# Optimization experiments

Measured on AMD Instinct MI355X. Metric: run time of the kernel, lower is better.

Reference implementation:

```python
import jax, jax.numpy as jnp
import numpy as np

B, D_IN, EMB = 8192, 4000, 96
H0, H1 = 2048, 1024
NB, NC, OPT = 8, 8, 32
NE = NB * NC  # 64 experts (total contests)


def setup_inputs() -> dict:
    key = jax.random.key(0)
    ks = jax.random.split(key, 10)
    scale = lambda fan_in: jnp.sqrt(2.0 / fan_in)  # kaiming_normal-ish
    return {
        "inputs": jax.random.normal(ks[0], (B, D_IN), dtype=jnp.float32),
        "emb_table": jax.random.normal(ks[1], (NE, EMB), dtype=jnp.float32) * scale(EMB),
        "W0": jax.random.normal(ks[2], (D_IN + EMB, H0), dtype=jnp.float32) * scale(D_IN + EMB),
        "b0": jnp.zeros((H0,), dtype=jnp.float32),
        "W1": jax.random.normal(ks[3], (H0, H1), dtype=jnp.float32) * scale(H0),
        "b1": jnp.zeros((H1,), dtype=jnp.float32),
        "We": jax.random.normal(ks[4], (NE, H1, OPT), dtype=jnp.float32) * scale(H1),
        "be": jnp.zeros((NE, OPT), dtype=jnp.float32),
        "ballot_number": jax.random.randint(ks[5], (B,), 0, NB, dtype=jnp.int32),
        "contest_number": jax.random.randint(ks[6], (B,), 0, NC, dtype=jnp.int32),
        "batches": B,
    }


def reference(inputs, emb_table, W0, b0, W1, b1, We, be,
              ballot_number, contest_number, batches):
    # flat expert index per sample: index_of[ballot][contest] with equal-size ballots
    expert = ballot_number * NC + contest_number                  # [B]
    x = inputs.reshape(batches, -1)                               # [B, D_IN]
    emb = emb_table[expert]                                       # [B, EMB] (gather)
    h = jnp.concatenate([emb, x], axis=1)                         # [B, D_IN+EMB]
    h = jax.nn.relu(h @ W0 + b0)                                  # fc0 (dropout = id at eval)
    h = jax.nn.relu(h @ W1 + b1)                                  # fc1
    # per-sample routed linear: gather expert weights, batched matvec
    out = jnp.einsum("bd,bdo->bo", h, We[expert]) + be[expert]    # [B, OPT]
    return jax.nn.sigmoid(out)
```

## Files before the change

### kernel.cpp

```cpp
#include <hip/hip_runtime.h>
#include <math.h>

typedef __attribute__((ext_vector_type(8))) short short8;
typedef __attribute__((ext_vector_type(4))) float f32x4;

#define B_SZ 8192
#define D_INN 4000
#define EMBD 96
#define H0D 2048
#define H1D 1024
#define KDIM 4096

__device__ __forceinline__ unsigned short f2bf(float f) {
  union { float f; unsigned u; } v; v.f = f;
  unsigned r = v.u + 0x7FFFu + ((v.u >> 16) & 1u);
  return (unsigned short)(r >> 16);
}
__device__ __forceinline__ float bf2f(unsigned short h) {
  union { unsigned u; float f; } v; v.u = ((unsigned)h) << 16;
  return v.f;
}
__device__ __forceinline__ void gld_lds16(const void* g, void* l) {
  __builtin_amdgcn_global_load_lds(
      (const __attribute__((address_space(1))) unsigned int*)g,
      (__attribute__((address_space(3))) unsigned int*)l, 16, 0, 0);
}

__global__ __launch_bounds__(256) void transpose_cvt(
    const float* __restrict__ in, unsigned short* __restrict__ out, int R, int C) {
  __shared__ float tile[32][33];
  int c0 = blockIdx.x * 32, r0 = blockIdx.y * 32;
  int tc = threadIdx.x & 31, tr = threadIdx.x >> 5;
#pragma unroll
  for (int i = 0; i < 4; ++i) {
    int r = tr + i * 8;
    tile[r][tc] = in[(size_t)(r0 + r) * C + (c0 + tc)];
  }
  __syncthreads();
#pragma unroll
  for (int i = 0; i < 4; ++i) {
    int rr = tr + i * 8;
    out[(size_t)(c0 + rr) * R + (r0 + tc)] = f2bf(tile[tc][rr]);
  }
}

__global__ __launch_bounds__(256) void build_A(
    const float* __restrict__ inputs, const float* __restrict__ emb,
    const int* __restrict__ ballot, const int* __restrict__ contest,
    unsigned short* __restrict__ A) {
  int gid = blockIdx.x * 256 + threadIdx.x;
  int b = gid >> 9, c = gid & 511;
  const float* src;
  if (c < EMBD / 8) {
    int e = ballot[b] * 8 + contest[b];
    src = emb + (size_t)e * EMBD + c * 8;
  } else {
    src = inputs + (size_t)b * D_INN + (c - EMBD / 8) * 8;
  }
  float4 v0 = *(const float4*)src;
  float4 v1 = *(const float4*)(src + 4);
  unsigned short r[8];
  r[0] = f2bf(v0.x); r[1] = f2bf(v0.y); r[2] = f2bf(v0.z); r[3] = f2bf(v0.w);
  r[4] = f2bf(v1.x); r[5] = f2bf(v1.y); r[6] = f2bf(v1.z); r[7] = f2bf(v1.w);
  *reinterpret_cast<short8*>(A + (size_t)b * KDIM + c * 8) =
      *reinterpret_cast<const short8*>(r);
}

template <int MREP>
__global__ __launch_bounds__(512, 2) void gemm_nt_pipe(
    const unsigned short* __restrict__ A, const unsigned short* __restrict__ Bt,
    const float* __restrict__ bias, unsigned short* __restrict__ C,
    int K, int N, int NBN) {
  constexpr int BM  = MREP * 32;
  constexpr int AI  = MREP / 4;
  constexpr int ASH = BM * 32;
  constexpr int MH  = MREP / 2;
  __shared__ unsigned short lds[3 * ASH + 3 * 8192];

  const int tid = threadIdx.x;
  const int w = tid >> 6, l = tid & 63;
  const int lr = l & 15, kg = l >> 4;
  const int wm = w >> 2, wn = w & 3;

  int swz = (blockIdx.x & 7) * ((int)gridDim.x >> 3) + ((int)blockIdx.x >> 3);
  const int bm = swz / NBN, bn = swz - bm * NBN;
  const int NT = K >> 5;

  const int rg = l >> 2;
  const int sl = ((l & 3) ^ ((l >> 3) & 3)) * 8;
  const unsigned short* ga[AI];
#pragma unroll
  for (int i = 0; i < AI; ++i)
    ga[i] = A + (size_t)(bm * BM + (i * 8 + w) * 16 + rg) * K + sl;
  const unsigned short* gb0 = Bt + (size_t)(bn * 256 + w * 16 + rg) * K + sl;
  const unsigned short* gb1 = gb0 + (size_t)128 * K;

  const int xo = (kg ^ ((lr >> 1) & 3)) << 4;
  const int aoff = (wm * (MREP * 16) + lr) * 64 + xo;
  const int boff = (wn * 64 + lr) * 64 + xo;

  f32x4 acc[MREP][4] = {};

  auto stageA = [&](int t, int rbuf) {
    unsigned short* la = lds + rbuf * ASH + w * 512;
    const int ko = t * 32;
#pragma unroll
    for (int i = 0; i < AI; ++i) gld_lds16(ga[i] + ko, la + i * 4096);
  };
  auto stageB = [&](int t, int rbuf) {
    unsigned short* lb = lds + 3 * ASH + rbuf * 8192 + w * 512;
    const int ko = t * 32;
    gld_lds16(gb0 + ko, lb);
    gld_lds16(gb1 + ko, lb + 4096);
  };

#define WAIT_VM_STEADY() do { \
    if constexpr (AI == 2) asm volatile("s_waitcnt vmcnt(4)" ::: "memory"); \
    else                   asm volatile("s_waitcnt vmcnt(3)" ::: "memory"); \
  } while (0)

  stageA(0, 0); stageB(0, 0);
  stageA(1, 1); stageB(1, 1);
  WAIT_VM_STEADY();
  __builtin_amdgcn_s_barrier();

  int rb = 0;
  for (int t = 0; t < NT; ++t) {
    int rb2 = rb + 2; if (rb2 >= 3) rb2 -= 3;
    const char* pa = (const char*)lds + rb * (ASH * 2) + aoff;
    const char* pb = (const char*)lds + 3 * (ASH * 2) + rb * 16384 + boff;

    short8 a0[MH], bfr[4];
#pragma unroll
    for (int mi = 0; mi < MH; ++mi) a0[mi] = *(const short8*)(pa + mi * 1024);
#pragma unroll
    for (int ni = 0; ni < 4; ++ni)  bfr[ni] = *(const short8*)(pb + ni * 1024);
    if (t + 2 < NT) stageA(t + 2, rb2);
    asm volatile("s_waitcnt lgkmcnt(0)" ::: "memory");
    __builtin_amdgcn_s_barrier();
    __builtin_amdgcn_s_setprio(1);
#pragma unroll
    for (int mi = 0; mi < MH; ++mi)
#pragma unroll
      for (int ni = 0; ni < 4; ++ni)
        acc[mi][ni] = __builtin_amdgcn_mfma_f32_16x16x32_bf16(
            a0[mi], bfr[ni], acc[mi][ni], 0, 0, 0);
    __builtin_amdgcn_s_setprio(0);

    short8 a1[MH];
#pragma unroll
    for (int mi = 0; mi < MH; ++mi) a1[mi] = *(const short8*)(pa + (MH + mi) * 1024);
    if (t + 2 < NT) {
      stageB(t + 2, rb2);
      asm volatile("s_waitcnt lgkmcnt(0)" ::: "memory");
      WAIT_VM_STEADY();
      __builtin_amdgcn_s_barrier();
    } else if (t + 1 < NT) {
      asm volatile("s_waitcnt lgkmcnt(0)" ::: "memory");
      asm volatile("s_waitcnt vmcnt(0)" ::: "memory");
      __builtin_amdgcn_s_barrier();
    } else {
      asm volatile("s_waitcnt lgkmcnt(0)" ::: "memory");
    }
    __builtin_amdgcn_s_setprio(1);
#pragma unroll
    for (int mi = 0; mi < MH; ++mi)
#pragma unroll
      for (int ni = 0; ni < 4; ++ni)
        acc[MH + mi][ni] = __builtin_amdgcn_mfma_f32_16x16x32_bf16(
            a1[mi], bfr[ni], acc[MH + mi][ni], 0, 0, 0);
    __builtin_amdgcn_s_setprio(0);

    rb = rb + 1; if (rb >= 3) rb = 0;
  }

#pragma unroll
  for (int mi = 0; mi < MREP; ++mi) {
    const int row0 = bm * BM + wm * (MREP * 16) + mi * 16 + kg * 4;
#pragma unroll
    for (int ni = 0; ni < 4; ++ni) {
      const int col = bn * 256 + wn * 64 + ni * 16 + lr;
      const float bv = bias[col];
#pragma unroll
      for (int j = 0; j < 4; ++j) {
        float v = acc[mi][ni][j] + bv;
        v = v > 0.f ? v : 0.f;
        C[(size_t)(row0 + j) * N + col] = f2bf(v);
      }
    }
  }
#undef WAIT_VM_STEADY
}

__global__ __launch_bounds__(256) void expert_head(
    const unsigned short* __restrict__ h1, const float* __restrict__ We,
    const float* __restrict__ be, const int* __restrict__ ballot,
    const int* __restrict__ contest, float* __restrict__ out) {
  int b = blockIdx.x * 4 + (threadIdx.x >> 6);
  int lane = threadIdx.x & 63;
  int o = lane & 31, half = lane >> 5;
  int e = ballot[b] * 8 + contest[b];
  const unsigned short* hrow = h1 + (size_t)b * H1D + half * 512;
  const float* wb = We + ((size_t)e * H1D + half * 512) * 32 + o;
  float acc = 0.f;
  for (int d0 = 0; d0 < 512; d0 += 8) {
    short8 hv = *reinterpret_cast<const short8*>(&hrow[d0]);
#pragma unroll
    for (int j = 0; j < 8; ++j)
      acc = fmaf(bf2f((unsigned short)hv[j]), wb[(size_t)(d0 + j) * 32], acc);
  }
  acc += __shfl_xor(acc, 32, 64);
  if (half == 0) {
    float x = acc + be[e * 32 + o];
    out[(size_t)b * 32 + o] = 1.f / (1.f + expf(-x));
  }
}

extern "C" void kernel_launch(void* const* d_in, const int* in_sizes, int n_in,
                              void* d_out, int out_size, void* d_ws, size_t ws_size,
                              hipStream_t stream) {
  const float* inputs = (const float*)d_in[0];
  const float* emb    = (const float*)d_in[1];
  const float* W0     = (const float*)d_in[2];
  const float* b0     = (const float*)d_in[3];
  const float* W1     = (const float*)d_in[4];
  const float* b1     = (const float*)d_in[5];
  const float* We     = (const float*)d_in[6];
  const float* be     = (const float*)d_in[7];
  const int* ballot   = (const int*)d_in[8];
  const int* contest  = (const int*)d_in[9];
  float* out = (float*)d_out;

  char* ws = (char*)d_ws;
  unsigned short* A   = (unsigned short*)(ws);
  unsigned short* W0t = (unsigned short*)(ws + 67108864);
  unsigned short* h0  = (unsigned short*)(ws + 83886080);
  unsigned short* W1t = (unsigned short*)(ws + 117440512);
  unsigned short* h1  = (unsigned short*)(ws + 121634816);

  dim3 blk(256);
  transpose_cvt<<<dim3(H0D / 32, KDIM / 32, 1), blk, 0, stream>>>(W0, W0t, KDIM, H0D);
  transpose_cvt<<<dim3(H1D / 32, H0D / 32, 1), blk, 0, stream>>>(W1, W1t, H0D, H1D);
  build_A<<<dim3(B_SZ * 512 / 256), blk, 0, stream>>>(inputs, emb, ballot, contest, A);
  gemm_nt_pipe<8><<<dim3((B_SZ / 256) * (H0D / 256)), dim3(512), 0, stream>>>(
      A, W0t, b0, h0, KDIM, H0D, H0D / 256);
  gemm_nt_pipe<4><<<dim3((B_SZ / 128) * (H1D / 256)), dim3(512), 0, stream>>>(
      h0, W1t, b1, h1, H0D, H1D, H1D / 256);
  expert_head<<<dim3(B_SZ / 4), blk, 0, stream>>>(h1, We, be, ballot, contest, out);
}
```

Before: 264.3 us.

## Add 8-phase ping-pong GEMM for fc0 and bucket expert head by expert

Replaces the fc0 GEMM with a new kernel that uses a 64-wide K step, double-buffered XOR-swizzled LDS, and four MFMA phases per K tile that interleave A and B half-tile loads, aiming for better load/compute overlap and fewer LDS bank conflicts. The expert head is rewritten to group samples per expert within quarter-batch chunks. Each group's h1 rows are staged in LDS and the expert's weights are reused across samples, rather than re-reading the gathered weights for every sample. The risks are the heavy 128 KB LDS use, one block per expert-quarter, and atomic-based bucketing that adds serial work per block.

```diff
diff --git a/kernel.cpp b/kernel.cpp
--- a/kernel.cpp
+++ b/kernel.cpp
@@ -66,8 +66,166 @@
       *reinterpret_cast<const short8*>(r);
 }
 
+#define BARRIER() __builtin_amdgcn_s_barrier()
+#define LGKM0() do { asm volatile("s_waitcnt lgkmcnt(0)" ::: "memory"); \
+                     __builtin_amdgcn_sched_barrier(0); } while (0)
+
+__global__ __launch_bounds__(512, 2) void gemm_nt_8ph(
+    const unsigned short* __restrict__ A, const unsigned short* __restrict__ Bt,
+    const float* __restrict__ bias, unsigned short* __restrict__ C,
+    int K, int N, int NBN) {
+  __shared__ char lds[131072];
+  const int tid = threadIdx.x;
+  const int w = tid >> 6, l = tid & 63;
+  const int lr = l & 15, kg = l >> 4;
+  const int wm = w >> 2, wn = w & 3;
+
+  int swz = (blockIdx.x & 7) * ((int)gridDim.x >> 3) + ((int)blockIdx.x >> 3);
+  const int bm = swz / NBN, bn = swz - bm * NBN;
+  const int NT = K >> 6;
+
+  const int row0 = w * 8 + (l >> 3);
+  const int ss8 = ((l & 7) ^ ((l >> 3) & 7)) * 8;
+  const unsigned short* gA[2] = {
+      A + (size_t)(bm * 256 + row0) * K + ss8,
+      A + (size_t)(bm * 256 + 128 + row0) * K + ss8 };
+  const unsigned short* gB[2] = {
+      Bt + (size_t)(bn * 256 + row0) * K + ss8,
+      Bt + (size_t)(bn * 256 + 128 + row0) * K + ss8 };
+
+  auto stage = [&](const unsigned short* gbase, int region, int h, int buf, int t) {
+    char* d = lds + region * 65536 + buf * 32768 + h * 16384 + w * 1024;
+    const unsigned short* s = gbase + (size_t)t * 64;
+    gld_lds16(s, d);
+    gld_lds16(s + (size_t)64 * K, d + 8192);
+  };
+
+  const int lswz = lr & 7;
+  auto rdA = [&](int buf, int mh, int mi, int kk) -> short8 {
+    const char* p = lds + buf * 32768 + wm * 16384 +
+        (mh * 64 + mi * 16 + lr) * 128 + ((((kk << 2) | kg)) ^ lswz) * 16;
+    return *(const short8*)p;
+  };
+  auto rdB = [&](int buf, int nh, int j, int kk) -> short8 {
+    const char* p = lds + 65536 + buf * 32768 + (wn >> 1) * 16384 +
+        ((wn & 1) * 64 + (nh * 2 + j) * 16 + lr) * 128 +
+        ((((kk << 2) | kg)) ^ lswz) * 16;
+    return *(const short8*)p;
+  };
+
+  f32x4 acc[8][4] = {};
+
+  stage(gB[1], 1, 1, 0, 0); stage(gA[0], 0, 0, 0, 0);
+  stage(gA[1], 0, 1, 0, 0); stage(gB[0], 1, 0, 0, 0);
+  stage(gB[1], 1, 1, 1, 1); stage(gA[0], 0, 0, 1, 1);
+  asm volatile("s_waitcnt vmcnt(4)" ::: "memory");
+  BARRIER();
+  __builtin_amdgcn_sched_barrier(0);
+
+  for (int t = 0; t < NT; ++t) {
+    const int buf = t & 1;
+    short8 a[4][2], a2[4][2], b[2][2], b2[2][2];
+
+#pragma unroll
+    for (int mi = 0; mi < 4; ++mi)
+#pragma unroll
+      for (int kk = 0; kk < 2; ++kk) a[mi][kk] = rdA(buf, 0, mi, kk);
+#pragma unroll
+    for (int j = 0; j < 2; ++j)
+#pragma unroll
+      for (int kk = 0; kk < 2; ++kk) b[j][kk] = rdB(buf, 0, j, kk);
+    if (t + 1 < NT) stage(gA[1], 0, 1, (t + 1) & 1, t + 1);
+    BARRIER(); LGKM0();
+    __builtin_amdgcn_s_setprio(1);
+#pragma unroll
+    for (int mi = 0; mi < 4; ++mi)
+#pragma unroll
+      for (int j = 0; j < 2; ++j)
+#pragma unroll
+        for (int kk = 0; kk < 2; ++kk)
+          acc[mi][j] = __builtin_amdgcn_mfma_f32_16x16x32_bf16(
+              a[mi][kk], b[j][kk], acc[mi][j], 0, 0, 0);
+    __builtin_amdgcn_s_setprio(0);
+    __builtin_amdgcn_sched_barrier(0);
+    BARRIER();
+
+#pragma unroll
+    for (int j = 0; j < 2; ++j)
+#pragma unroll
+      for (int kk = 0; kk < 2; ++kk) b2[j][kk] = rdB(buf, 1, j, kk);
+    if (t + 1 < NT) stage(gB[0], 1, 0, (t + 1) & 1, t + 1);
+    BARRIER(); LGKM0();
+    __builtin_amdgcn_s_setprio(1);
+#pragma unroll
+    for (int mi = 0; mi < 4; ++mi)
+#pragma unroll
+      for (int j = 0; j < 2; ++j)
+#pragma unroll
+        for (int kk = 0; kk < 2; ++kk)
+          acc[mi][2 + j] = __builtin_amdgcn_mfma_f32_16x16x32_bf16(
+              a[mi][kk], b2[j][kk], acc[mi][2 + j], 0, 0, 0);
+    __builtin_amdgcn_s_setprio(0);
+    __builtin_amdgcn_sched_barrier(0);
+    BARRIER();
+
+#pragma unroll
+    for (int mi = 0; mi < 4; ++mi)
+#pragma unroll
+      for (int kk = 0; kk < 2; ++kk) a2[mi][kk] = rdA(buf, 1, mi, kk);
+    if (t + 2 < NT) stage(gB[1], 1, 1, buf, t + 2);
+    BARRIER(); LGKM0();
+    __builtin_amdgcn_s_setprio(1);
+#pragma unroll
+    for (int mi = 0; mi < 4; ++mi)
+#pragma unroll
+      for (int j = 0; j < 2; ++j)
+#pragma unroll
+        for (int kk = 0; kk < 2; ++kk)
+          acc[4 + mi][2 + j] = __builtin_amdgcn_mfma_f32_16x16x32_bf16(
+              a2[mi][kk], b2[j][kk], acc[4 + mi][2 + j], 0, 0, 0);
+    __builtin_amdgcn_s_setprio(0);
+    __builtin_amdgcn_sched_barrier(0);
+    BARRIER();
+
+    if (t + 2 < NT) stage(gA[0], 0, 0, buf, t + 2);
+    __builtin_amdgcn_s_setprio(1);
+#pragma unroll
+    for (int mi = 0; mi < 4; ++mi)
+#pragma unroll
+      for (int j = 0; j < 2; ++j)
+#pragma unroll
+        for (int kk = 0; kk < 2; ++kk)
+          acc[4 + mi][j] = __builtin_amdgcn_mfma_f32_16x16x32_bf16(
+              a2[mi][kk], b[j][kk], acc[4 + mi][j], 0, 0, 0);
+    __builtin_amdgcn_s_setprio(0);
+    __builtin_amdgcn_sched_barrier(0);
+    if (t + 1 < NT) {
+      if (t + 2 < NT) asm volatile("s_waitcnt vmcnt(4)" ::: "memory");
+      else            asm volatile("s_waitcnt vmcnt(0)" ::: "memory");
+      BARRIER();
+    }
+    __builtin_amdgcn_sched_barrier(0);
+  }
+
+#pragma unroll
+  for (int mi = 0; mi < 8; ++mi) {
+    const int row0w = bm * 256 + wm * 128 + mi * 16 + kg * 4;
+#pragma unroll
+    for (int ni = 0; ni < 4; ++ni) {
+      const int col = bn * 256 + wn * 64 + ni * 16 + lr;
+      const float bv = bias[col];
+#pragma unroll
+      for (int j = 0; j < 4; ++j) {
+        float v = acc[mi][ni][j] + bv;
+        v = v > 0.f ? v : 0.f;
+        C[(size_t)(row0w + j) * N + col] = f2bf(v);
+      }
+    }
+  }
+}
+
 template <int MREP>
-__global__ __launch_bounds__(512, 2) void gemm_nt_pipe(
+__global__ __launch_bounds__(512, 2) void gemm_nt_2ph(
     const unsigned short* __restrict__ A, const unsigned short* __restrict__ Bt,
     const float* __restrict__ bias, unsigned short* __restrict__ C,
     int K, int N, int NBN) {
@@ -122,7 +280,7 @@
   stageA(0, 0); stageB(0, 0);
   stageA(1, 1); stageB(1, 1);
   WAIT_VM_STEADY();
-  __builtin_amdgcn_s_barrier();
+  BARRIER();
 
   int rb = 0;
   for (int t = 0; t < NT; ++t) {
@@ -137,7 +295,7 @@
     for (int ni = 0; ni < 4; ++ni)  bfr[ni] = *(const short8*)(pb + ni * 1024);
     if (t + 2 < NT) stageA(t + 2, rb2);
     asm volatile("s_waitcnt lgkmcnt(0)" ::: "memory");
-    __builtin_amdgcn_s_barrier();
+    BARRIER();
     __builtin_amdgcn_s_setprio(1);
 #pragma unroll
     for (int mi = 0; mi < MH; ++mi)
@@ -154,11 +312,11 @@
       stageB(t + 2, rb2);
       asm volatile("s_waitcnt lgkmcnt(0)" ::: "memory");
       WAIT_VM_STEADY();
-      __builtin_amdgcn_s_barrier();
+      BARRIER();
     } else if (t + 1 < NT) {
       asm volatile("s_waitcnt lgkmcnt(0)" ::: "memory");
       asm volatile("s_waitcnt vmcnt(0)" ::: "memory");
-      __builtin_amdgcn_s_barrier();
+      BARRIER();
     } else {
       asm volatile("s_waitcnt lgkmcnt(0)" ::: "memory");
     }
@@ -192,27 +350,54 @@
 #undef WAIT_VM_STEADY
 }
 
-__global__ __launch_bounds__(256) void expert_head(
+__global__ __launch_bounds__(256) void expert_head_bucketed(
     const unsigned short* __restrict__ h1, const float* __restrict__ We,
     const float* __restrict__ be, const int* __restrict__ ballot,
     const int* __restrict__ contest, float* __restrict__ out) {
-  int b = blockIdx.x * 4 + (threadIdx.x >> 6);
-  int lane = threadIdx.x & 63;
-  int o = lane & 31, half = lane >> 5;
-  int e = ballot[b] * 8 + contest[b];
-  const unsigned short* hrow = h1 + (size_t)b * H1D + half * 512;
-  const float* wb = We + ((size_t)e * H1D + half * 512) * 32 + o;
-  float acc = 0.f;
-  for (int d0 = 0; d0 < 512; d0 += 8) {
-    short8 hv = *reinterpret_cast<const short8*>(&hrow[d0]);
-#pragma unroll
-    for (int j = 0; j < 8; ++j)
-      acc = fmaf(bf2f((unsigned short)hv[j]), wb[(size_t)(d0 + j) * 32], acc);
-  }
-  acc += __shfl_xor(acc, 32, 64);
-  if (half == 0) {
-    float x = acc + be[e * 32 + o];
-    out[(size_t)b * 32 + o] = 1.f / (1.f + expf(-x));
+  const int e = blockIdx.x >> 2, q = blockIdx.x & 3;
+  __shared__ unsigned short sidx[2048];
+  __shared__ int scnt;
+  __shared__ unsigned short sh1[32][1032];
+  if (threadIdx.x == 0) scnt = 0;
+  __syncthreads();
+  const int base = q * 2048;
+  for (int i = threadIdx.x; i < 2048; i += 256) {
+    int s = base + i;
+    if (ballot[s] * 8 + contest[s] == e)
+      sidx[atomicAdd(&scnt, 1)] = (unsigned short)s;
+  }
+  __syncthreads();
+  const int cnt = scnt;
+  const int so = threadIdx.x >> 3;
+  const int oq = threadIdx.x & 7;
+  const float4* We4 = (const float4*)(We + (size_t)e * H1D * 32);
+  for (int c0 = 0; c0 < cnt; c0 += 32) {
+    const int ns = min(32, cnt - c0);
+    __syncthreads();
+    for (int t = threadIdx.x; t < ns * 128; t += 256) {
+      int r = t >> 7, cc = (t & 127) * 8;
+      *(short8*)&sh1[r][cc] =
+          *(const short8*)&h1[(size_t)sidx[c0 + r] * H1D + cc];
+    }
+    __syncthreads();
+    if (so < ns) {
+      const int s = sidx[c0 + so];
+      float ax = 0.f, ay = 0.f, az = 0.f, aw = 0.f;
+#pragma unroll 8
+      for (int d = 0; d < H1D; ++d) {
+        float h = bf2f(sh1[so][d]);
+        float4 wv = We4[d * 8 + oq];
+        ax = fmaf(h, wv.x, ax); ay = fmaf(h, wv.y, ay);
+        az = fmaf(h, wv.z, az); aw = fmaf(h, wv.w, aw);
+      }
+      float4 bb = *(const float4*)&be[e * 32 + oq * 4];
+      float4 r;
+      r.x = 1.f / (1.f + expf(-(ax + bb.x)));
+      r.y = 1.f / (1.f + expf(-(ay + bb.y)));
+      r.z = 1.f / (1.f + expf(-(az + bb.z)));
+      r.w = 1.f / (1.f + expf(-(aw + bb.w)));
+      *(float4*)&out[(size_t)s * 32 + oq * 4] = r;
+    }
   }
 }
 
@@ -242,9 +427,7 @@
   transpose_cvt<<<dim3(H0D / 32, KDIM / 32, 1), blk, 0, stream>>>(W0, W0t, KDIM, H0D);
   transpose_cvt<<<dim3(H1D / 32, H0D / 32, 1), blk, 0, stream>>>(W1, W1t, H0D, H1D);
   build_A<<<dim3(B_SZ * 512 / 256), blk, 0, stream>>>(inputs, emb, ballot, contest, A);
-  gemm_nt_pipe<8><<<dim3((B_SZ / 256) * (H0D / 256)), dim3(512), 0, stream>>>(
-      A, W0t, b0, h0, KDIM, H0D, H0D / 256);
-  gemm_nt_pipe<4><<<dim3((B_SZ / 128) * (H1D / 256)), dim3(512), 0, stream>>>(
-      h0, W1t, b1, h1, H0D, H1D, H1D / 256);
-  expert_head<<<dim3(B_SZ / 4), blk, 0, stream>>>(h1, We, be, ballot, contest, out);
-}
+  gemm_nt_8ph<<<dim3(256), dim3(512), 0, stream>>>(A, W0t, b0, h0, KDIM, H0D, H0D / 256);
+  gemm_nt_2ph<4><<<dim3(256), dim3(512), 0, stream>>>(h0, W1t, b1, h1, H0D, H1D, H1D / 256);
+  expert_head_bucketed<<<dim3(256), blk, 0, stream>>>(h1, We, be, ballot, contest, out);
+}
```

Measured after the change: 288.7 us. 1.09x slower.
